# Performance work log

Hardware: AMD Instinct MI355X
Metric: run time of the kernel (lower is better)

## Reference

```python
import jax, jax.numpy as jnp
import numpy as np

B = 262144      # points per batch
DIM = 3         # input_dim
L = 16          # levels
T = 19          # log2 hash table size
F = 2           # features per level
N_MIN, N_MAX = 16, 512

_b = np.exp((np.log(N_MAX) - np.log(N_MIN)) / (L - 1))
RES = np.floor(N_MIN * _b ** np.arange(L)).astype(np.float32).reshape(1, 1, L, 1)

# voxel corner offsets [1, DIM, 1, 2^DIM]
_border = np.empty((DIM, 2 ** DIM), dtype=np.uint32)
for i in range(DIM):
    _border[i, :] = np.array(([0] * 2 ** i + [1] * 2 ** i) * 2 ** (DIM - i - 1), dtype=np.uint32)
BORDER = _border.reshape(1, DIM, 1, 2 ** DIM)

# tiny-cuda-nn hash primes; all fit in uint32. Since the torch code takes the
# result mod 2^T (a power of two), int64 and uint32 arithmetic agree on the
# low bits, so uint32 hashing is bit-exact with the original.
PRIMES = np.array([1, 2654435761, 805459861], dtype=np.uint32)
MASK = np.uint32(2 ** T - 1)


def setup_inputs() -> dict:
    key = jax.random.key(0)
    k1, k2 = jax.random.split(key)
    x = jax.random.uniform(k1, (B, DIM), dtype=jnp.float32)  # coords in [0,1)
    tables = jax.random.uniform(k2, (L, 2 ** T, F), dtype=jnp.float32,
                                minval=-1e-4, maxval=1e-4)
    return {"x": x, "tables": tables}


def reference(x, tables):
    res = jnp.asarray(RES)                                   # [1,1,L,1]
    border = jnp.asarray(BORDER)                             # [1,DIM,1,2^DIM]
    primes = jnp.asarray(PRIMES)
    scaled = x[:, :, None, None] * res                       # [B,DIM,L,1]
    grid = jnp.floor(scaled).astype(jnp.uint32) + border     # [B,DIM,L,2^DIM]
    # spatial hash: xor of per-dim coord * prime, mod 2^T
    h = (grid[:, 0] * primes[0]) ^ (grid[:, 1] * primes[1]) ^ (grid[:, 2] * primes[2])
    idx = (h & MASK).astype(jnp.int32)                       # [B,L,2^DIM]
    gathered = tables[jnp.arange(L)[None, :, None], idx]     # [B,L,2^DIM,F]
    # multilinear interpolation weights
    w = jnp.prod(1.0 - jnp.abs(scaled - grid.astype(scaled.dtype)), axis=1)  # [B,L,2^DIM]
    out = jnp.einsum('blv,blvf->blf', w, gathered)           # [B,L,F]
    return out.reshape(x.shape[0], L * F)
```

## Files before the change

### kernel.cpp

```cpp
#include <hip/hip_runtime.h>


#define NB 262144
#define NL 16
#define TSIZE (1u << 19)
#define TMASK ((1u << 19) - 1u)
#define P1 2654435761u
#define P2 805459861u

#define NCL 3
#define CPTS 8192
#define COARSE_BLOCKS 256
#define CLDS_ENT (17 * 17 * 17)
#define FINE_CHUNKS 512
#define FINE_TOTAL ((NL - NCL) * FINE_CHUNKS)
#define FINE_PER_XCD (FINE_TOTAL / 8)
#define GRID_BLOCKS (COARSE_BLOCKS + FINE_TOTAL)

typedef float vf2 __attribute__((ext_vector_type(2)));
typedef float vf4 __attribute__((ext_vector_type(4)));

__constant__ float RES_C[NL] = {16.f, 20.f, 25.f, 32.f, 40.f, 50.f, 64.f, 80.f,
                                101.f, 128.f, 161.f, 203.f, 256.f, 322.f, 406.f, 512.f};

__device__ __forceinline__ void ngp_point_level(
    float px, float py, float pz, int l, const float* __restrict__ tables,
    float& o0, float& o1) {
  const float res = RES_C[l];
  const float sx = px * res, sy = py * res, sz = pz * res;
  const float fx = floorf(sx), fy = floorf(sy), fz = floorf(sz);
  const unsigned ix = (unsigned)fx, iy = (unsigned)fy, iz = (unsigned)fz;

  const unsigned hy0 = iy * P1, hy1 = hy0 + P1;
  const unsigned hz0 = iz * P2, hz1 = hz0 + P2;

  const float wx0 = 1.0f - fabsf(sx - fx);
  const float wx1 = 1.0f - fabsf(sx - (fx + 1.0f));
  const float wy0 = 1.0f - fabsf(sy - fy);
  const float wy1 = 1.0f - fabsf(sy - (fy + 1.0f));
  const float wz0 = 1.0f - fabsf(sz - fz);
  const float wz1 = 1.0f - fabsf(sz - (fz + 1.0f));

  const vf2* __restrict__ tbl2 = (const vf2*)tables + (size_t)l * TSIZE;
  const vf4* __restrict__ tbl4 = (const vf4*)tables + (size_t)l * (TSIZE / 2);

  unsigned hyz[4];
  hyz[0] = hy0 ^ hz0;
  hyz[1] = hy1 ^ hz0;
  hyz[2] = hy0 ^ hz1;
  hyz[3] = hy1 ^ hz1;

  vf2 g[8];
  if ((ix & 1u) == 0u) {
#pragma unroll
    for (int p = 0; p < 4; ++p) {
      const unsigned i0 = (ix ^ hyz[p]) & TMASK;
      const vf4 q = tbl4[i0 >> 1];
      vf2 lo; lo.x = q.x; lo.y = q.y;
      vf2 hi; hi.x = q.z; hi.y = q.w;
      const bool x0_is_lo = (i0 & 1u) == 0u;
      g[2 * p + 0] = x0_is_lo ? lo : hi;
      g[2 * p + 1] = x0_is_lo ? hi : lo;
    }
  } else {
#pragma unroll
    for (int p = 0; p < 4; ++p) {
      const unsigned i0 = (ix ^ hyz[p]) & TMASK;
      const unsigned i1 = ((ix + 1u) ^ hyz[p]) & TMASK;
      g[2 * p + 0] = tbl2[i0];
      g[2 * p + 1] = tbl2[i1];
    }
  }

  o0 = 0.0f; o1 = 0.0f;
#pragma unroll
  for (int v = 0; v < 8; ++v) {
    const float w = ((v & 1) ? wx1 : wx0) * ((v & 2) ? wy1 : wy0) * ((v & 4) ? wz1 : wz0);
    o0 = fmaf(w, g[v].x, o0);
    o1 = fmaf(w, g[v].y, o1);
  }
}

template <int E, int PLANES>
__device__ __forceinline__ void coarse_slab(
    const int lvl, const int zbase, const int c_lo, const int c_hi,
    const int cchunk, const float* __restrict__ x,
    const float* __restrict__ tables, vf2* __restrict__ ws,
    vf2* __restrict__ cache) {
  const int tid = threadIdx.x;
  const vf4* __restrict__ tbl4 = (const vf4*)tables + (size_t)lvl * (TSIZE / 2);

  constexpr int HE = (E + 1) / 2;
  constexpr int U = HE * E * PLANES;

  for (int u = tid; u < U; u += 512) {
    const int zp = u / (HE * E);
    const int rem = u - zp * (HE * E);
    const int iy = rem / HE;
    const int ixh = rem - iy * HE;
    const unsigned ix = 2u * (unsigned)ixh;
    const unsigned iz = (unsigned)(zbase + zp);
    const unsigned h0 = (ix ^ ((unsigned)iy * P1) ^ (iz * P2)) & TMASK;
    const vf4 q = tbl4[h0 >> 1];
    vf2 lo; lo.x = q.x; lo.y = q.y;
    vf2 hi; hi.x = q.z; hi.y = q.w;
    const bool x0_is_lo = (h0 & 1u) == 0u;
    const int d0 = (int)ix + E * iy + E * E * zp;
    cache[d0] = x0_is_lo ? lo : hi;
    if ((int)ix + 1 < E) cache[d0 + 1] = x0_is_lo ? hi : lo;
  }
  __syncthreads();

  const float res = RES_C[lvl];
  const int base = cchunk * CPTS;
#pragma unroll
  for (int k = 0; k < CPTS / 512; ++k) {
    const int b = base + k * 512 + tid;
    const float px = x[b * 3 + 0];
    const float py = x[b * 3 + 1];
    const float pz = x[b * 3 + 2];

    const float sx = px * res, sy = py * res, sz = pz * res;
    const float fx = floorf(sx), fy = floorf(sy), fz = floorf(sz);
    const int ix = (int)fx, iy = (int)fy, iz = (int)fz;

    if (iz >= c_lo && iz <= c_hi) {
      const float wx0 = 1.0f - fabsf(sx - fx);
      const float wx1 = 1.0f - fabsf(sx - (fx + 1.0f));
      const float wy0 = 1.0f - fabsf(sy - fy);
      const float wy1 = 1.0f - fabsf(sy - (fy + 1.0f));
      const float wz0 = 1.0f - fabsf(sz - fz);
      const float wz1 = 1.0f - fabsf(sz - (fz + 1.0f));

      const int d = ix + E * iy + E * E * (iz - zbase);
      vf2 g[8];
      g[0] = cache[d];
      g[1] = cache[d + 1];
      g[2] = cache[d + E];
      g[3] = cache[d + E + 1];
      g[4] = cache[d + E * E];
      g[5] = cache[d + E * E + 1];
      g[6] = cache[d + E * E + E];
      g[7] = cache[d + E * E + E + 1];

      float o0 = 0.0f, o1 = 0.0f;
#pragma unroll
      for (int v = 0; v < 8; ++v) {
        const float w = ((v & 1) ? wx1 : wx0) * ((v & 2) ? wy1 : wy0) * ((v & 4) ? wz1 : wz0);
        o0 = fmaf(w, g[v].x, o0);
        o1 = fmaf(w, g[v].y, o1);
      }
      vf2 r; r.x = o0; r.y = o1;
      __builtin_nontemporal_store(r, ws + (size_t)lvl * NB + b);
    }
  }
}

__global__ __launch_bounds__(512, 8) void ngp_gather3(
    const float* __restrict__ x,
    const float* __restrict__ tables,
    vf2* __restrict__ ws) {
  __shared__ vf2 cache[CLDS_ENT];

  const int bid = blockIdx.x;
  if (bid < COARSE_BLOCKS) {
    if (bid < 32) {
      coarse_slab<17, 17>(0, 0, 0, 15, bid, x, tables, ws, cache);
    } else if (bid < 96) {
      const int u = bid - 32;
      const int half = u >> 5;
      coarse_slab<21, 11>(1, half * 10, half * 10, half * 10 + 9, u & 31,
                          x, tables, ws, cache);
    } else {
      const int u = bid - 96;
      const int s = u >> 5;
      coarse_slab<26, 6>(2, 5 * s, 5 * s, 5 * s + 4, u & 31,
                         x, tables, ws, cache);
    }
    return;
  }

  const int fid = bid - COARSE_BLOCKS;
  const int x8 = fid & 7;
  const int j = fid >> 3;
  const int g = x8 * FINE_PER_XCD + j;
  const int lvl = NCL + (g >> 9);
  const int b = (g & 511) * 512 + threadIdx.x;

  const float px = __builtin_nontemporal_load(x + b * 3 + 0);
  const float py = __builtin_nontemporal_load(x + b * 3 + 1);
  const float pz = __builtin_nontemporal_load(x + b * 3 + 2);

  float o0, o1;
  ngp_point_level(px, py, pz, lvl, tables, o0, o1);

  vf2 r; r.x = o0; r.y = o1;
  __builtin_nontemporal_store(r, ws + (size_t)lvl * NB + b);
}

__global__ __launch_bounds__(256) void ngp_transpose_kernel(
    const vf2* __restrict__ ws,
    vf4* __restrict__ out4) {
  __shared__ vf2 tile[NL][257];
  const int t = threadIdx.x;
  const int p0 = blockIdx.x * 256;

#pragma unroll
  for (int l = 0; l < NL; ++l) {
    tile[l][t] = __builtin_nontemporal_load(ws + (size_t)l * NB + p0 + t);
  }
  __syncthreads();

#pragma unroll
  for (int k = 0; k < 8; ++k) {
    const int q = k * 256 + t;
    const int pq = q >> 3;
    const int wq = q & 7;
    const vf2 a = tile[2 * wq + 0][pq];
    const vf2 c = tile[2 * wq + 1][pq];
    vf4 v; v.x = a.x; v.y = a.y; v.z = c.x; v.w = c.y;
    __builtin_nontemporal_store(v, out4 + (size_t)p0 * 8 + q);
  }
}

__global__ __launch_bounds__(256) void ngp_fused_kernel(
    const float* __restrict__ x, const float* __restrict__ tables,
    float* __restrict__ out) {
  const int tid = blockIdx.x * blockDim.x + threadIdx.x;
  const int l = tid & (NL - 1);
  const int b = tid >> 4;
  float o0, o1;
  ngp_point_level(x[b * 3], x[b * 3 + 1], x[b * 3 + 2], l, tables, o0, o1);
  float2 r = make_float2(o0, o1);
  ((float2*)out)[tid] = r;
}

extern "C" void kernel_launch(void* const* d_in, const int* in_sizes, int n_in,
                              void* d_out, int out_size, void* d_ws, size_t ws_size,
                              hipStream_t stream) {
  const float* x = (const float*)d_in[0];
  const float* tables = (const float*)d_in[1];
  float* out = (float*)d_out;

  const size_t ws_needed = (size_t)NL * NB * sizeof(vf2);
  if (ws_size >= ws_needed) {
    vf2* ws = (vf2*)d_ws;
    ngp_gather3<<<GRID_BLOCKS, 512, 0, stream>>>(x, tables, ws);
    ngp_transpose_kernel<<<NB / 256, 256, 0, stream>>>(ws, (vf4*)out);
  } else {
    ngp_fused_kernel<<<NB * NL / 256, 256, 0, stream>>>(x, tables, out);
  }
}
```

Measured before the change: 190.2 us.

## Fuse gather and transpose into cooperative persistent kernel with dense mid-level grids

Replaces the two-kernel gather plus transpose with one cooperative persistent kernel that has three phases separated by grid syncs. Phase one builds dense, unhashed corner grids in workspace for levels 3 to 6 so those levels can read two corners with one 16-byte load instead of scattered hashed gathers. Phase two hands out coarse and fine work items through per-XCD atomic counters, and phase three does the level-to-point transpose in the same kernel. The gains are fewer launches and better locality, paid for by two grid-wide barriers, extra workspace and a dense prebuild on every call.

New measurement: 350.7 us. 84.4% more time.

```diff
diff --git a/kernel.cpp b/kernel.cpp
--- a/kernel.cpp
+++ b/kernel.cpp
@@ -1,4 +1,7 @@
 #include <hip/hip_runtime.h>
+#include <hip/hip_cooperative_groups.h>
+
+namespace cg = cooperative_groups;
 
 
 #define NB 262144
@@ -10,18 +13,32 @@
 
 #define NCL 3
 #define CPTS 8192
-#define COARSE_BLOCKS 256
 #define CLDS_ENT (17 * 17 * 17)
-#define FINE_CHUNKS 512
-#define FINE_TOTAL ((NL - NCL) * FINE_CHUNKS)
-#define FINE_PER_XCD (FINE_TOTAL / 8)
-#define GRID_BLOCKS (COARSE_BLOCKS + FINE_TOTAL)
+
+#define E3 33
+#define E4 41
+#define E5 51
+#define E6 65
+#define DOFF3 0
+#define DOFF4 35944
+#define DOFF5 104872
+#define DOFF6 237528
+#define DENSE_TOTAL 512160
+
+#define FC1 18513
+#define FC2 53814
+#define FC3 121440
+#define FTOTAL 260865
+
+#define FINE_TOTAL 6656
 
 typedef float vf2 __attribute__((ext_vector_type(2)));
 typedef float vf4 __attribute__((ext_vector_type(4)));
 
 __constant__ float RES_C[NL] = {16.f, 20.f, 25.f, 32.f, 40.f, 50.f, 64.f, 80.f,
                                 101.f, 128.f, 161.f, 203.f, 256.f, 322.f, 406.f, 512.f};
+
+__constant__ int XSPLIT[9] = {0, 1099, 2150, 2901, 3652, 4403, 5154, 5905, 6656};
 
 __device__ __forceinline__ void ngp_point_level(
     float px, float py, float pz, int l, const float* __restrict__ tables,
@@ -81,6 +98,42 @@
   }
 }
 
+template <int E, int DOFF_>
+__device__ __forceinline__ void dense_point(
+    float px, float py, float pz, float res, const vf2* __restrict__ dense,
+    float& o0, float& o1) {
+  const float sx = px * res, sy = py * res, sz = pz * res;
+  const float fx = floorf(sx), fy = floorf(sy), fz = floorf(sz);
+  const int ix = (int)fx, iy = (int)fy, iz = (int)fz;
+
+  const float wx0 = 1.0f - fabsf(sx - fx);
+  const float wx1 = 1.0f - fabsf(sx - (fx + 1.0f));
+  const float wy0 = 1.0f - fabsf(sy - fy);
+  const float wy1 = 1.0f - fabsf(sy - (fy + 1.0f));
+  const float wz0 = 1.0f - fabsf(sz - fz);
+  const float wz1 = 1.0f - fabsf(sz - (fz + 1.0f));
+
+  const vf2* __restrict__ dp = dense + DOFF_ + ix + E * iy + E * E * iz;
+
+  vf2 g[8];
+#pragma unroll
+  for (int p = 0; p < 4; ++p) {
+    const int row = ((p & 1) ? E : 0) + ((p & 2) ? E * E : 0);
+    vf4 q;
+    __builtin_memcpy(&q, (const void*)(dp + row), 16);
+    g[2 * p + 0].x = q.x; g[2 * p + 0].y = q.y;
+    g[2 * p + 1].x = q.z; g[2 * p + 1].y = q.w;
+  }
+
+  o0 = 0.0f; o1 = 0.0f;
+#pragma unroll
+  for (int v = 0; v < 8; ++v) {
+    const float w = ((v & 1) ? wx1 : wx0) * ((v & 2) ? wy1 : wy0) * ((v & 4) ? wz1 : wz0);
+    o0 = fmaf(w, g[v].x, o0);
+    o1 = fmaf(w, g[v].y, o1);
+  }
+}
+
 template <int E, int PLANES>
 __device__ __forceinline__ void coarse_slab(
     const int lvl, const int zbase, const int c_lo, const int c_hi,
@@ -93,6 +146,7 @@
   constexpr int HE = (E + 1) / 2;
   constexpr int U = HE * E * PLANES;
 
+  __syncthreads();
   for (int u = tid; u < U; u += 512) {
     const int zp = u / (HE * E);
     const int rem = u - zp * (HE * E);
@@ -156,9 +210,131 @@
   }
 }
 
+__global__ __launch_bounds__(512, 8) void ngp_coop(
+    const float* __restrict__ x, const float* __restrict__ tables,
+    vf2* __restrict__ ws, float* __restrict__ out) {
+  __shared__ vf2 smem[CLDS_ENT];
+  __shared__ int s_item;
+  const int tid = threadIdx.x;
+  const int bid = blockIdx.x;
+  const int nblk = gridDim.x;
+
+  vf2* __restrict__ dense = ws + (size_t)NL * NB;
+  unsigned* ctr = (unsigned*)(dense + DENSE_TOTAL);
+
+  {
+    const int gtid = bid * 512 + tid;
+    if (gtid < 8) ctr[gtid] = 0u;
+    for (int u = gtid; u < FTOTAL; u += nblk * 512) {
+      int lv, E, doff, ubase;
+      if (u < FC1)      { lv = 0; E = E3; doff = DOFF3; ubase = 0; }
+      else if (u < FC2) { lv = 1; E = E4; doff = DOFF4; ubase = FC1; }
+      else if (u < FC3) { lv = 2; E = E5; doff = DOFF5; ubase = FC2; }
+      else              { lv = 3; E = E6; doff = DOFF6; ubase = FC3; }
+      const int ul = u - ubase;
+      const int HE = (E + 1) >> 1;
+      const int plane = HE * E;
+      const int iz = ul / plane;
+      const int rem = ul - iz * plane;
+      const int iy = rem / HE;
+      const int ixh = rem - iy * HE;
+      const unsigned ix = 2u * (unsigned)ixh;
+      const unsigned h0 = (ix ^ ((unsigned)iy * P1) ^ ((unsigned)iz * P2)) & TMASK;
+      const vf4* __restrict__ tbl4 =
+          (const vf4*)tables + (size_t)(NCL + lv) * (TSIZE / 2);
+      const vf4 q = tbl4[h0 >> 1];
+      vf2 lo; lo.x = q.x; lo.y = q.y;
+      vf2 hi; hi.x = q.z; hi.y = q.w;
+      const bool el = (h0 & 1u) == 0u;
+      const int d0 = doff + (int)ix + E * iy + E * E * iz;
+      dense[d0] = el ? lo : hi;
+      if ((int)ix + 1 < E) dense[d0 + 1] = el ? hi : lo;
+    }
+  }
+  cg::this_grid().sync();
+
+  {
+    const int x8 = bid & 7;
+    const int c0 = XSPLIT[x8], c1 = XSPLIT[x8 + 1];
+    const int nitems = 32 + (c1 - c0);
+    for (;;) {
+      if (tid == 0) s_item = (int)atomicAdd(&ctr[x8], 1u);
+      __syncthreads();
+      const int it = s_item;
+      __syncthreads();
+      if (it >= nitems) break;
+
+      if (it < 32) {
+        const int g = it * 8 + x8;
+        if (g < 32) {
+          coarse_slab<17, 17>(0, 0, 0, 15, g, x, tables, ws, smem);
+        } else if (g < 96) {
+          const int u = g - 32;
+          const int hf = u >> 5;
+          coarse_slab<21, 11>(1, hf * 10, hf * 10, hf * 10 + 9, u & 31,
+                              x, tables, ws, smem);
+        } else {
+          const int u = g - 96;
+          const int s = u >> 5;
+          coarse_slab<26, 6>(2, 5 * s, 5 * s, 5 * s + 4, u & 31,
+                             x, tables, ws, smem);
+        }
+      } else {
+        const int c = c0 + (it - 32);
+        const int lvl = NCL + (c >> 9);
+        const int b = (c & 511) * 512 + tid;
+
+        const float px = __builtin_nontemporal_load(x + b * 3 + 0);
+        const float py = __builtin_nontemporal_load(x + b * 3 + 1);
+        const float pz = __builtin_nontemporal_load(x + b * 3 + 2);
+
+        float o0, o1;
+        if (lvl < 7) {
+          switch (lvl) {
+            case 3:  dense_point<E3, DOFF3>(px, py, pz, RES_C[3], dense, o0, o1); break;
+            case 4:  dense_point<E4, DOFF4>(px, py, pz, RES_C[4], dense, o0, o1); break;
+            case 5:  dense_point<E5, DOFF5>(px, py, pz, RES_C[5], dense, o0, o1); break;
+            default: dense_point<E6, DOFF6>(px, py, pz, RES_C[6], dense, o0, o1); break;
+          }
+        } else {
+          ngp_point_level(px, py, pz, lvl, tables, o0, o1);
+        }
+        vf2 r; r.x = o0; r.y = o1;
+        __builtin_nontemporal_store(r, ws + (size_t)lvl * NB + b);
+      }
+    }
+  }
+  cg::this_grid().sync();
+
+  {
+    vf2 (*tile)[257] = (vf2(*)[257])smem;
+    vf4* __restrict__ out4 = (vf4*)out;
+    for (int t = bid; t < NB / 256; t += nblk) {
+      __syncthreads();
+      const int p0 = t * 256;
+      for (int u = tid; u < NL * 256; u += 512) {
+        const int l = u >> 8, p = u & 255;
+        tile[l][p] = __builtin_nontemporal_load(ws + (size_t)l * NB + p0 + p);
+      }
+      __syncthreads();
+      for (int u = tid; u < 2048; u += 512) {
+        const int pq = u >> 3;
+        const int wq = u & 7;
+        const vf2 a = tile[2 * wq + 0][pq];
+        const vf2 c = tile[2 * wq + 1][pq];
+        vf4 v; v.x = a.x; v.y = a.y; v.z = c.x; v.w = c.y;
+        __builtin_nontemporal_store(v, out4 + (size_t)p0 * 8 + u);
+      }
+    }
+  }
+}
+
+#define COARSE_BLOCKS 256
+#define FINE_PER_XCD (FINE_TOTAL / 8)
+#define GRID_BLOCKS (COARSE_BLOCKS + FINE_TOTAL)
+
 __global__ __launch_bounds__(512, 8) void ngp_gather3(
-    const float* __restrict__ x,
-    const float* __restrict__ tables,
+    const float* __restrict__ x, const float* __restrict__ tables,
     vf2* __restrict__ ws) {
   __shared__ vf2 cache[CLDS_ENT];
 
@@ -199,8 +375,7 @@
 }
 
 __global__ __launch_bounds__(256) void ngp_transpose_kernel(
-    const vf2* __restrict__ ws,
-    vf4* __restrict__ out4) {
+    const vf2* __restrict__ ws, vf4* __restrict__ out4) {
   __shared__ vf2 tile[NL][257];
   const int t = threadIdx.x;
   const int p0 = blockIdx.x * 256;
@@ -242,8 +417,47 @@
   const float* tables = (const float*)d_in[1];
   float* out = (float*)d_out;
 
-  const size_t ws_needed = (size_t)NL * NB * sizeof(vf2);
-  if (ws_size >= ws_needed) {
+  const size_t ws_basic = (size_t)NL * NB * sizeof(vf2);
+  const size_t ws_coop = ws_basic + (size_t)DENSE_TOTAL * 8 + 64;
+
+  if (ws_size >= ws_coop) {
+    static int nblk = 0;
+    if (nblk == 0) {
+      int occ = 0;
+      hipError_t e =
+          hipOccupancyMaxActiveBlocksPerMultiprocessor(&occ, ngp_coop, 512, 0);
+      int ncu = 256;
+      hipDeviceProp_t prop;
+      int dev = 0;
+      hipGetDevice(&dev);
+      if (hipGetDeviceProperties(&prop, dev) == hipSuccess &&
+          prop.multiProcessorCount > 0)
+        ncu = prop.multiProcessorCount;
+      if (e != hipSuccess || occ <= 0) {
+        nblk = -1;
+      } else {
+        int bpc = occ > 4 ? 4 : occ;
+        int nb = bpc * ncu;
+        nb -= nb % 8;
+        nblk = nb > 0 ? nb : -1;
+      }
+    }
+    if (nblk > 0) {
+      vf2* ws = (vf2*)d_ws;
+      const float* xa = x;
+      const float* ta = tables;
+      vf2* wsa = ws;
+      float* outa = out;
+      void* args[4] = {&xa, &ta, &wsa, &outa};
+      if (hipLaunchCooperativeKernel(ngp_coop, dim3(nblk), dim3(512), args, 0,
+                                     stream) == hipSuccess) {
+        return;
+      }
+      nblk = -1;
+    }
+  }
+
+  if (ws_size >= ws_basic) {
     vf2* ws = (vf2*)d_ws;
     ngp_gather3<<<GRID_BLOCKS, 512, 0, stream>>>(x, tables, ws);
     ngp_transpose_kernel<<<NB / 256, 256, 0, stream>>>(ws, (vf4*)out);
```
